# Performance work log

Hardware: AMD Instinct MI355X
Metric: run time of the kernel (lower is better)

The kernel has to match this reference:

```python
import jax, jax.numpy as jnp
import numpy as np
import math

NUM_HEADS = 16
SEGMENT_SIZE = 256
DILATION_RATE = 2


def _hilbert_curve(n):
    if n == 1:
        return [(0, 0)]
    m = n // 2
    sub = _hilbert_curve(m)
    pts = [(y, x) for (x, y) in sub]
    pts += [(x, y + m) for (x, y) in sub]
    pts += [(x + m, y + m) for (x, y) in sub]
    pts += [(m - 1 - y + m, m - 1 - x) for (x, y) in sub]
    return pts


def generate_hilbert_curve_mapping(seq_len):
    grid = 2 ** int(math.ceil(math.log2(math.sqrt(seq_len))))
    pts = _hilbert_curve(grid)
    lin2hil = np.zeros(seq_len, dtype=np.int32)
    for h_idx, (x, y) in enumerate(pts[:seq_len]):
        lin = y * grid + x
        if lin < seq_len:
            lin2hil[lin] = h_idx
    return lin2hil


def setup_inputs() -> dict:
    key = jax.random.key(0)
    k1, k2, k3 = jax.random.split(key, 3)
    B, S, H = 1, 4096, 2048
    scale = H ** -0.5
    x = jax.random.normal(k1, (B, S, H), dtype=jnp.float32)
    w_qkv = jax.random.normal(k2, (3 * H, H), dtype=jnp.float32) * scale
    w_out = jax.random.normal(k3, (H, H), dtype=jnp.float32) * scale
    hilbert_map = jnp.asarray(generate_hilbert_curve_mapping(S))
    return {"x": x, "w_qkv": w_qkv, "w_out": w_out, "hilbert_map": hilbert_map}


def _kv_positions(S, seg, dil):
    # Union of per-segment dilated positions: seg_start + j*dil (< segment end).
    seg_starts = np.arange(0, S, seg)
    within = np.arange(0, seg, dil)
    return jnp.asarray((seg_starts[:, None] + within[None, :]).reshape(-1))


def reference(x, w_qkv, w_out, hilbert_map):
    B, S, H = x.shape
    nh = NUM_HEADS
    hd = H // nh
    qkv = x @ w_qkv.T                              # [B,S,3H]
    qkv = qkv.reshape(B, S, 3, nh, hd).transpose(2, 0, 3, 1, 4)  # [3,B,nh,S,hd]
    q, k, v = qkv[0], qkv[1], qkv[2]

    kv_pos = _kv_positions(S, SEGMENT_SIZE, DILATION_RATE)  # [Nk]
    gathered = hilbert_map[kv_pos]                 # Hilbert-mapped KV indices
    kg = k[:, :, gathered, :]                      # [B,nh,Nk,hd]
    vg = v[:, :, gathered, :]

    scale = 1.0 / jnp.sqrt(jnp.float32(hd))
    scores = jnp.einsum("bhmd,bhnd->bhmn", q, kg) * scale
    p = jax.nn.softmax(scores, axis=-1)
    acc = jnp.einsum("bhmn,bhnd->bhmd", p, vg)     # [B,nh,S,hd]

    # Scatter: out[:, :, hilbert_map[m], :] = acc[:, :, m, :]
    out = jnp.zeros_like(acc).at[:, :, hilbert_map, :].set(acc)
    out = out.transpose(0, 2, 1, 3).reshape(B, S, H)
    return out @ w_out.T
```

## Files before the change

### kernel.cpp

```cpp
#include <hip/hip_runtime.h>
#include <math.h>

#define S_LEN 4096
#define HID   2048
#define NH    16
#define HD    128
#define NKV   2048
#define KT    64
#define QBLK  128
#define NT    (NKV / KT)
#define QSCALE 0.12754103668587426f

typedef __attribute__((ext_vector_type(8))) _Float16 half8;
typedef __attribute__((ext_vector_type(4))) _Float16 half4;
typedef __attribute__((ext_vector_type(2))) __fp16 fp16x2;
typedef __attribute__((ext_vector_type(4))) float f32x4;
typedef __attribute__((ext_vector_type(16))) float f32x16;

#define GLB_AS __attribute__((address_space(1)))
#define LDS_AS __attribute__((address_space(3)))

#if __has_builtin(__builtin_amdgcn_exp2f)
#define EXP2(x) __builtin_amdgcn_exp2f(x)
#else
#define EXP2(x) exp2f(x)
#endif

__device__ __forceinline__ void gload16(const void* g, void* l) {
  __builtin_amdgcn_global_load_lds((GLB_AS const void*)g, (LDS_AS void*)l, 16, 0, 0);
}

__device__ __forceinline__ unsigned pkrtz(float a, float b) {
  union { fp16x2 h; unsigned u; } cv;
  cv.h = __builtin_amdgcn_cvt_pkrtz(a, b);
  return cv.u;
}

__global__ void k_build_idx(const int* __restrict__ hmap, int* __restrict__ gidx) {
  int i = blockIdx.x * 256 + threadIdx.x;
  if (i < NKV) gidx[i] = hmap[2 * i];
}

#define NX8  (S_LEN * HID / 8)
#define NW8  (3 * HID * HID / 8)
#define NO8  (HID * HID / 8)
__global__ void k_cvt_all(const float* __restrict__ x, const float* __restrict__ wq,
                          const float* __restrict__ wo, _Float16* __restrict__ x16,
                          _Float16* __restrict__ wq16, _Float16* __restrict__ wo16) {
  int i = blockIdx.x * 256 + threadIdx.x;
  const float* src; _Float16* dst; int j;
  if (i < NX8)            { src = x;  dst = x16;  j = i; }
  else if (i < NX8 + NW8) { src = wq; dst = wq16; j = i - NX8; }
  else                    { src = wo; dst = wo16; j = i - NX8 - NW8; }
  float4 a = ((const float4*)src)[2 * j];
  float4 b = ((const float4*)src)[2 * j + 1];
  half8 h;
  h[0] = (_Float16)a.x; h[1] = (_Float16)a.y; h[2] = (_Float16)a.z; h[3] = (_Float16)a.w;
  h[4] = (_Float16)b.x; h[5] = (_Float16)b.y; h[6] = (_Float16)b.z; h[7] = (_Float16)b.w;
  ((half8*)dst)[j] = h;
}

__global__ __launch_bounds__(256)
void k_gemm_qkv(const _Float16* __restrict__ A, const _Float16* __restrict__ wqkv,
                _Float16* __restrict__ q16, const int* __restrict__ gidx,
                char* __restrict__ kimg, char* __restrict__ vtimg)
{
  __shared__ __align__(16) char Asl[16384];
  __shared__ __align__(16) char Bsl[16384];
  const int tid = threadIdx.x;
  const int w = tid >> 6, lane = tid & 63;
  const int l15 = lane & 15, l4 = lane >> 4;
  const int wr = w >> 1, wc = w & 1;
  const int K = HID;

  int b = blockIdx.x;
  const bool qpart = b < 512;
  int m0, n0, N;
  const _Float16* B;
  const int* arow;
  if (qpart) { m0 = (b >> 4) * 128; n0 = (b & 15) * 128; N = HID; B = wqkv; arow = nullptr; }
  else { b -= 512; m0 = (b >> 5) * 128; n0 = (b & 31) * 128; N = 2 * HID;
         B = wqkv + (size_t)HID * HID; arow = gidx; }

  const int srow  = lane >> 3;
  const int kso   = ((lane & 7) ^ srow) * 8;
  const _Float16* Ap[4];
  const _Float16* Bp[4];
#pragma unroll
  for (int q = 0; q < 4; ++q) {
    int arel = m0 + 32 * w + 8 * q + srow;
    int ra = arow ? arow[arel] : arel;
    Ap[q] = A + (size_t)ra * K + kso;
    Bp[q] = B + (size_t)(n0 + 32 * w + 8 * q + srow) * K + kso;
  }

  f32x4 acc[4][4];
#pragma unroll
  for (int i = 0; i < 4; ++i)
#pragma unroll
    for (int j = 0; j < 4; ++j) acc[i][j] = (f32x4){0.f, 0.f, 0.f, 0.f};

#define STAGE_T(k0)                                                  \
  do {                                                               \
    _Pragma("unroll")                                                \
    for (int q = 0; q < 4; ++q) {                                    \
      gload16(Ap[q] + (k0), Asl + (4 * w + q) * 1024 + lane * 16);   \
      gload16(Bp[q] + (k0), Bsl + (4 * w + q) * 1024 + lane * 16);   \
    }                                                                \
  } while (0)

  STAGE_T(0);
  __syncthreads();

  const int nt = K >> 6;
  for (int t = 0; t < nt; ++t) {
    half8 af[4][2], bf[4][2];
#pragma unroll
    for (int mi = 0; mi < 4; ++mi) {
      int row = wr * 64 + mi * 16 + l15;
#pragma unroll
      for (int ks = 0; ks < 2; ++ks)
        af[mi][ks] = *(const half8*)(Asl + row * 128 + (((ks * 4 + l4) ^ (row & 7)) * 16));
    }
#pragma unroll
    for (int ni = 0; ni < 4; ++ni) {
      int row = wc * 64 + ni * 16 + l15;
#pragma unroll
      for (int ks = 0; ks < 2; ++ks)
        bf[ni][ks] = *(const half8*)(Bsl + row * 128 + (((ks * 4 + l4) ^ (row & 7)) * 16));
    }
    __syncthreads();
    if (t + 1 < nt) STAGE_T((t + 1) * 64);
    __builtin_amdgcn_s_setprio(1);
#pragma unroll
    for (int mi = 0; mi < 4; ++mi)
#pragma unroll
      for (int ni = 0; ni < 4; ++ni)
#pragma unroll
        for (int ks = 0; ks < 2; ++ks)
          acc[mi][ni] = __builtin_amdgcn_mfma_f32_16x16x32_f16(af[mi][ks], bf[ni][ks], acc[mi][ni], 0, 0, 0);
    __builtin_amdgcn_s_setprio(0);
    __syncthreads();
  }
#undef STAGE_T

  const int rbase = m0 + wr * 64 + l4 * 4;
  const int cbase = n0 + wc * 64 + l15;
#pragma unroll
  for (int mi = 0; mi < 4; ++mi)
#pragma unroll
    for (int ni = 0; ni < 4; ++ni)
#pragma unroll
      for (int e = 0; e < 4; ++e) {
        int row = rbase + mi * 16 + e;
        int col = cbase + ni * 16;
        _Float16 val = (_Float16)acc[mi][ni][e];
        if (qpart) {
          q16[(size_t)row * HID + col] = val;
        } else {
          int t = row >> 6, j = row & 63;
          if (col < HID) {
            int h = col >> 7, d = col & 127;
            int off = (h * 32 + t) * 16384 + ((j * 256 + 2 * d) ^ ((j & 7) << 4));
            *(_Float16*)(kimg + off) = val;
          } else {
            int nn = col - HID;
            int h = nn >> 7, d = nn & 127;
            int off = (h * 32 + t) * 16384 + ((d * 128 + 2 * j) ^ ((d & 7) << 4));
            *(_Float16*)(vtimg + off) = val;
          }
        }
      }
}

__global__ __launch_bounds__(256)
void k_gemm_out(const _Float16* __restrict__ A, const _Float16* __restrict__ B,
                float* __restrict__ C, int M, int N, int K)
{
  __shared__ __align__(16) char Asl[16384];
  __shared__ __align__(16) char Bsl[16384];
  const int tid = threadIdx.x;
  const int w = tid >> 6, lane = tid & 63;
  const int l15 = lane & 15, l4 = lane >> 4;
  const int m0 = blockIdx.y * 128, n0 = blockIdx.x * 128;
  const int wr = w >> 1, wc = w & 1;

  const int srow  = lane >> 3;
  const int kso   = ((lane & 7) ^ srow) * 8;
  const _Float16* Ap[4];
  const _Float16* Bp[4];
#pragma unroll
  for (int q = 0; q < 4; ++q) {
    int row = m0 + 32 * w + 8 * q + srow;
    Ap[q] = A + (size_t)row * K + kso;
    Bp[q] = B + (size_t)(n0 + 32 * w + 8 * q + srow) * K + kso;
  }

  f32x4 acc[4][4];
#pragma unroll
  for (int i = 0; i < 4; ++i)
#pragma unroll
    for (int j = 0; j < 4; ++j) acc[i][j] = (f32x4){0.f, 0.f, 0.f, 0.f};

#define STAGE_T(k0)                                                  \
  do {                                                               \
    _Pragma("unroll")                                                \
    for (int q = 0; q < 4; ++q) {                                    \
      gload16(Ap[q] + (k0), Asl + (4 * w + q) * 1024 + lane * 16);   \
      gload16(Bp[q] + (k0), Bsl + (4 * w + q) * 1024 + lane * 16);   \
    }                                                                \
  } while (0)

  STAGE_T(0);
  __syncthreads();

  const int nt = K >> 6;
  for (int t = 0; t < nt; ++t) {
    half8 af[4][2], bf[4][2];
#pragma unroll
    for (int mi = 0; mi < 4; ++mi) {
      int row = wr * 64 + mi * 16 + l15;
#pragma unroll
      for (int ks = 0; ks < 2; ++ks)
        af[mi][ks] = *(const half8*)(Asl + row * 128 + (((ks * 4 + l4) ^ (row & 7)) * 16));
    }
#pragma unroll
    for (int ni = 0; ni < 4; ++ni) {
      int row = wc * 64 + ni * 16 + l15;
#pragma unroll
      for (int ks = 0; ks < 2; ++ks)
        bf[ni][ks] = *(const half8*)(Bsl + row * 128 + (((ks * 4 + l4) ^ (row & 7)) * 16));
    }
    __syncthreads();
    if (t + 1 < nt) STAGE_T((t + 1) * 64);
    __builtin_amdgcn_s_setprio(1);
#pragma unroll
    for (int mi = 0; mi < 4; ++mi)
#pragma unroll
      for (int ni = 0; ni < 4; ++ni)
#pragma unroll
        for (int ks = 0; ks < 2; ++ks)
          acc[mi][ni] = __builtin_amdgcn_mfma_f32_16x16x32_f16(af[mi][ks], bf[ni][ks], acc[mi][ni], 0, 0, 0);
    __builtin_amdgcn_s_setprio(0);
    __syncthreads();
  }
#undef STAGE_T

  const int rbase = m0 + wr * 64 + l4 * 4;
  const int cbase = n0 + wc * 64 + l15;
#pragma unroll
  for (int mi = 0; mi < 4; ++mi)
#pragma unroll
    for (int ni = 0; ni < 4; ++ni)
#pragma unroll
      for (int e = 0; e < 4; ++e)
        C[(size_t)(rbase + mi * 16 + e) * N + cbase + ni * 16] = acc[mi][ni][e];
}

__global__ __launch_bounds__(256, 2)
void k_attn9(const _Float16* __restrict__ qmat, const char* __restrict__ kimg,
             const char* __restrict__ vtimg, const int* __restrict__ hmap,
             _Float16* __restrict__ att)
{
  extern __shared__ __align__(16) char lds[];
  const int tid = threadIdx.x;
  const int w = tid >> 6, lane = tid & 63;
  const int l31 = lane & 31;
  const bool hi = (lane >> 5) != 0;
  const int hib = hi ? 1 : 0;
  const int work = (blockIdx.x & 7) * 64 + (blockIdx.x >> 3);
  const int h  = work >> 5;
  const int q0 = (work & 31) * QBLK;

  half8 qf[8];
  {
    const int qrow = q0 + w * 32 + l31;
    const _Float16* qb = qmat + (size_t)qrow * HID + h * HD + hib * 8;
    const _Float16 qs = (_Float16)QSCALE;
#pragma unroll
    for (int dk = 0; dk < 8; ++dk) {
      half8 v = *(const half8*)(qb + 16 * dk);
#pragma unroll
      for (int q = 0; q < 8; ++q) v[q] *= qs;
      qf[dk] = v;
    }
  }

  const int swz = (l31 & 7) << 4;
  int koff[4], voff[4];
#pragma unroll
  for (int i = 0; i < 4; ++i) {
    koff[i] = l31 * 256 + ((i * 32 + hib * 16) ^ swz);
    voff[i] = 16384 + l31 * 128 + ((i * 32 + hib * 16) ^ swz);
  }

  const char* kbase = kimg  + (size_t)h * NT * 16384;
  const char* vbase = vtimg + (size_t)h * NT * 16384;

  f32x16 acc[4];
#pragma unroll
  for (int dt = 0; dt < 4; ++dt)
#pragma unroll
    for (int r = 0; r < 16; ++r) acc[dt][r] = 0.f;
  float lsum = 0.f;

#define STAGE(buf, t)                                                          \
  do {                                                                         \
    const char* ks_ = kbase + (size_t)(t) * 16384;                             \
    const char* vs_ = vbase + (size_t)(t) * 16384;                             \
    char* d_ = lds + (buf) * 32768;                                            \
    _Pragma("unroll")                                                          \
    for (int g = 0; g < 4; ++g) {                                              \
      gload16(ks_ + (w + 4 * g) * 1024 + lane * 16, d_ + (w + 4 * g) * 1024);  \
      gload16(vs_ + (w + 4 * g) * 1024 + lane * 16,                            \
              d_ + 16384 + (w + 4 * g) * 1024);                                \
    }                                                                          \
  } while (0)

#define SM_HALF(S, PPK)                                                        \
  do {                                                                         \
    float p_[16];                                                              \
    _Pragma("unroll")                                                          \
    for (int r = 0; r < 16; ++r) { p_[r] = EXP2((S)[r]); lsum += p_[r]; }      \
    _Pragma("unroll")                                                          \
    for (int rq = 0; rq < 4; ++rq)                                             \
      _Pragma("unroll")                                                        \
      for (int h2 = 0; h2 < 2; ++h2)                                           \
        PPK[rq][h2] = pkrtz(p_[4 * rq + 2 * h2], p_[4 * rq + 2 * h2 + 1]);     \
  } while (0)

#define PV_HALF(PPK, KSB, CUR)                                                 \
  do {                                                                         \
    _Pragma("unroll")                                                          \
    for (int k1 = 0; k1 < 2; ++k1) {                                           \
      unsigned send0 = hi ? PPK[2 * k1][0]     : PPK[2 * k1 + 1][0];           \
      unsigned send1 = hi ? PPK[2 * k1][1]     : PPK[2 * k1 + 1][1];           \
      unsigned recv0 = (unsigned)__shfl_xor((int)send0, 32);                   \
      unsigned recv1 = (unsigned)__shfl_xor((int)send1, 32);                   \
      unsigned self0 = hi ? PPK[2 * k1 + 1][0] : PPK[2 * k1][0];               \
      unsigned self1 = hi ? PPK[2 * k1 + 1][1] : PPK[2 * k1][1];               \
      union { unsigned u[4]; half8 hv; } pf;                                   \
      pf.u[0] = hi ? recv0 : self0;                                            \
      pf.u[1] = hi ? recv1 : self1;                                            \
      pf.u[2] = hi ? self0 : recv0;                                            \
      pf.u[3] = hi ? self1 : recv1;                                            \
      __builtin_amdgcn_s_setprio(1);                                           \
      _Pragma("unroll")                                                        \
      for (int dt = 0; dt < 4; ++dt) {                                         \
        half8 vf = *(const half8*)(lds + voff[(KSB) + k1] +                    \
                    ((CUR) * 32768 + dt * 4096));                              \
        acc[dt] = __builtin_amdgcn_mfma_f32_32x32x16_f16(vf, pf.hv, acc[dt], 0, 0, 0); \
      }                                                                        \
      __builtin_amdgcn_s_setprio(0);                                           \
    }                                                                          \
  } while (0)

#define QK_HALF(S, JT, CUR)                                                    \
  do {                                                                         \
    _Pragma("unroll")                                                          \
    for (int r = 0; r < 16; ++r) (S)[r] = 0.f;                                 \
    __builtin_amdgcn_s_setprio(1);                                             \
    _Pragma("unroll")                                                          \
    for (int dk = 0; dk < 8; ++dk) {                                           \
      half8 kf = *(const half8*)(lds + koff[dk & 3] +                          \
                  ((CUR) * 32768 + (JT) * 8192 + (dk >> 2) * 128));            \
      (S) = __builtin_amdgcn_mfma_f32_32x32x16_f16(kf, qf[dk], (S), 0, 0, 0);  \
    }                                                                          \
    __builtin_amdgcn_s_setprio(0);                                             \
  } while (0)

#define TILE(CUR, T)                                                           \
  do {                                                                         \
    if ((T) + 1 < NT) STAGE((CUR) ^ 1, (T) + 1);                               \
    f32x16 sA, sB;                                                             \
    QK_HALF(sA, 0, CUR);                                                       \
    QK_HALF(sB, 1, CUR);                                                       \
    unsigned PA[4][2], PB[4][2];                                               \
    SM_HALF(sA, PA);                                                           \
    PV_HALF(PA, 0, CUR);                                                       \
    SM_HALF(sB, PB);                                                           \
    PV_HALF(PB, 2, CUR);                                                       \
    asm volatile("s_waitcnt vmcnt(0)");                                        \
    __syncthreads();                                                           \
  } while (0)

  STAGE(0, 0);
  asm volatile("s_waitcnt vmcnt(0)");
  __syncthreads();

  for (int t = 0; t < NT; t += 2) {
    TILE(0, t);
    TILE(1, t + 1);
  }
#undef TILE
#undef QK_HALF
#undef PV_HALF
#undef SM_HALF
#undef STAGE

  float lt = lsum + __shfl_xor(lsum, 32);
  const float rl = 1.0f / lt;
  const int qrow = q0 + w * 32 + l31;
  const int srow = hmap[qrow];
  _Float16* ob = att + (size_t)srow * HID + h * HD;
#pragma unroll
  for (int dt = 0; dt < 4; ++dt)
#pragma unroll
    for (int rq = 0; rq < 4; ++rq) {
      const int d0 = dt * 32 + 8 * rq + 4 * hib;
      half4 o;
      o[0] = (_Float16)(acc[dt][4 * rq + 0] * rl);
      o[1] = (_Float16)(acc[dt][4 * rq + 1] * rl);
      o[2] = (_Float16)(acc[dt][4 * rq + 2] * rl);
      o[3] = (_Float16)(acc[dt][4 * rq + 3] * rl);
      *(half4*)(ob + d0) = o;
    }
}

extern "C" void kernel_launch(void* const* d_in, const int* in_sizes, int n_in,
                              void* d_out, int out_size, void* d_ws, size_t ws_size,
                              hipStream_t stream)
{
  const float* x     = (const float*)d_in[0];
  const float* w_qkv = (const float*)d_in[1];
  const float* w_out = (const float*)d_in[2];
  const int*   hmap  = (const int*)d_in[3];
  float* out = (float*)d_out;

  char* ws = (char*)d_ws;
  int* gidx = (int*)ws;                                          ws += 8192;
  _Float16* x16    = (_Float16*)ws;
  _Float16* att16  = (_Float16*)ws;                              ws += (size_t)S_LEN * HID * 2;
  _Float16* wqkv16 = (_Float16*)ws;                              ws += (size_t)3 * HID * HID * 2;
  _Float16* wout16 = (_Float16*)ws;                              ws += (size_t)HID * HID * 2;
  _Float16* q16    = (_Float16*)ws;                              ws += (size_t)S_LEN * HID * 2;
  char* kimg  = ws;                                              ws += (size_t)NH * NT * 16384;
  char* vtimg = ws;

  k_build_idx<<<8, 256, 0, stream>>>(hmap, gidx);
  k_cvt_all<<<(NX8 + NW8 + NO8 + 255) / 256, 256, 0, stream>>>(x, w_qkv, w_out,
                                                               x16, wqkv16, wout16);

  k_gemm_qkv<<<1024, 256, 0, stream>>>(x16, wqkv16, q16, gidx, kimg, vtimg);

  k_attn9<<<NH * (S_LEN / QBLK), 256, 65536, stream>>>(q16, kimg, vtimg, hmap, att16);

  dim3 go(HID / 128, S_LEN / 128);
  k_gemm_out<<<go, 256, 0, stream>>>(att16, wout16, out, S_LEN, HID, HID);
}
```

Before: 224.5 us.

## Use 512-thread attention blocks with 4-stage KV ring and software-pipelined QK

The attention kernel now runs 8 waves per block over 256 query rows, so each staged K/V tile is shared by twice as many queries. The LDS double buffer becomes a four-slot ring that prefetches three tiles ahead, with partial vmcnt waits. The QK product for the next tile is interleaved with softmax and PV of the current tile to overlap MFMA work. This needs 128KB of LDS per block, which with launch_bounds(512,2) may limit residency and increase register pressure from the extra in-flight score tiles.

```diff
diff --git a/kernel.cpp b/kernel.cpp
--- a/kernel.cpp
+++ b/kernel.cpp
@@ -7,7 +7,7 @@
 #define HD    128
 #define NKV   2048
 #define KT    64
-#define QBLK  128
+#define QBLK  256
 #define NT    (NKV / KT)
 #define QSCALE 0.12754103668587426f
 
@@ -257,10 +257,10 @@
         C[(size_t)(rbase + mi * 16 + e) * N + cbase + ni * 16] = acc[mi][ni][e];
 }
 
-__global__ __launch_bounds__(256, 2)
-void k_attn9(const _Float16* __restrict__ qmat, const char* __restrict__ kimg,
-             const char* __restrict__ vtimg, const int* __restrict__ hmap,
-             _Float16* __restrict__ att)
+__global__ __launch_bounds__(512, 2)
+void k_attn10(const _Float16* __restrict__ qmat, const char* __restrict__ kimg,
+              const char* __restrict__ vtimg, const int* __restrict__ hmap,
+              _Float16* __restrict__ att)
 {
   extern __shared__ __align__(16) char lds[];
   const int tid = threadIdx.x;
@@ -268,9 +268,9 @@
   const int l31 = lane & 31;
   const bool hi = (lane >> 5) != 0;
   const int hib = hi ? 1 : 0;
-  const int work = (blockIdx.x & 7) * 64 + (blockIdx.x >> 3);
-  const int h  = work >> 5;
-  const int q0 = (work & 31) * QBLK;
+  const int work = (blockIdx.x & 7) * 32 + (blockIdx.x >> 3);
+  const int h  = work >> 4;
+  const int q0 = (work & 15) * QBLK;
 
   half8 qf[8];
   {
@@ -309,12 +309,10 @@
     const char* ks_ = kbase + (size_t)(t) * 16384;                             \
     const char* vs_ = vbase + (size_t)(t) * 16384;                             \
     char* d_ = lds + (buf) * 32768;                                            \
-    _Pragma("unroll")                                                          \
-    for (int g = 0; g < 4; ++g) {                                              \
-      gload16(ks_ + (w + 4 * g) * 1024 + lane * 16, d_ + (w + 4 * g) * 1024);  \
-      gload16(vs_ + (w + 4 * g) * 1024 + lane * 16,                            \
-              d_ + 16384 + (w + 4 * g) * 1024);                                \
-    }                                                                          \
+    gload16(ks_ + w * 1024 + lane * 16,          d_ + w * 1024);               \
+    gload16(ks_ + (8 + w) * 1024 + lane * 16,    d_ + (8 + w) * 1024);         \
+    gload16(vs_ + w * 1024 + lane * 16,          d_ + 16384 + w * 1024);       \
+    gload16(vs_ + (8 + w) * 1024 + lane * 16,    d_ + 16384 + (8 + w) * 1024); \
   } while (0)
 
 #define SM_HALF(S, PPK)                                                        \
@@ -329,7 +327,7 @@
         PPK[rq][h2] = pkrtz(p_[4 * rq + 2 * h2], p_[4 * rq + 2 * h2 + 1]);     \
   } while (0)
 
-#define PV_HALF(PPK, KSB, CUR)                                                 \
+#define PV_HALF(PPK, KSB, BUF)                                                 \
   do {                                                                         \
     _Pragma("unroll")                                                          \
     for (int k1 = 0; k1 < 2; ++k1) {                                           \
@@ -348,14 +346,14 @@
       _Pragma("unroll")                                                        \
       for (int dt = 0; dt < 4; ++dt) {                                         \
         half8 vf = *(const half8*)(lds + voff[(KSB) + k1] +                    \
-                    ((CUR) * 32768 + dt * 4096));                              \
+                    ((BUF) * 32768 + dt * 4096));                              \
         acc[dt] = __builtin_amdgcn_mfma_f32_32x32x16_f16(vf, pf.hv, acc[dt], 0, 0, 0); \
       }                                                                        \
       __builtin_amdgcn_s_setprio(0);                                           \
     }                                                                          \
   } while (0)
 
-#define QK_HALF(S, JT, CUR)                                                    \
+#define QK_HALF(S, JT, BUF)                                                    \
   do {                                                                         \
     _Pragma("unroll")                                                          \
     for (int r = 0; r < 16; ++r) (S)[r] = 0.f;                                 \
@@ -363,35 +361,46 @@
     _Pragma("unroll")                                                          \
     for (int dk = 0; dk < 8; ++dk) {                                           \
       half8 kf = *(const half8*)(lds + koff[dk & 3] +                          \
-                  ((CUR) * 32768 + (JT) * 8192 + (dk >> 2) * 128));            \
+                  ((BUF) * 32768 + (JT) * 8192 + (dk >> 2) * 128));            \
       (S) = __builtin_amdgcn_mfma_f32_32x32x16_f16(kf, qf[dk], (S), 0, 0, 0);  \
     }                                                                          \
     __builtin_amdgcn_s_setprio(0);                                             \
   } while (0)
 
-#define TILE(CUR, T)                                                           \
+#define TILE(CUR, T, DOSTAGE, DOQK, WAITASM)                                   \
   do {                                                                         \
-    if ((T) + 1 < NT) STAGE((CUR) ^ 1, (T) + 1);                               \
-    f32x16 sA, sB;                                                             \
-    QK_HALF(sA, 0, CUR);                                                       \
-    QK_HALF(sB, 1, CUR);                                                       \
+    if (DOSTAGE) STAGE((((CUR) + 3) & 3), (T) + 3);                            \
     unsigned PA[4][2], PB[4][2];                                               \
     SM_HALF(sA, PA);                                                           \
-    PV_HALF(PA, 0, CUR);                                                       \
+    if (DOQK) QK_HALF(sA, 0, (((CUR) + 1) & 3));                               \
+    PV_HALF(PA, 0, (CUR));                                                     \
     SM_HALF(sB, PB);                                                           \
-    PV_HALF(PB, 2, CUR);                                                       \
-    asm volatile("s_waitcnt vmcnt(0)");                                        \
-    __syncthreads();                                                           \
+    if (DOQK) QK_HALF(sB, 1, (((CUR) + 1) & 3));                               \
+    PV_HALF(PB, 2, (CUR));                                                     \
+    asm volatile(WAITASM ::: "memory");                                        \
+    __builtin_amdgcn_s_barrier();                                              \
   } while (0)
 
   STAGE(0, 0);
-  asm volatile("s_waitcnt vmcnt(0)");
-  __syncthreads();
-
-  for (int t = 0; t < NT; t += 2) {
-    TILE(0, t);
-    TILE(1, t + 1);
-  }
+  STAGE(1, 1);
+  STAGE(2, 2);
+  asm volatile("s_waitcnt vmcnt(4)" ::: "memory");
+  __builtin_amdgcn_s_barrier();
+
+  f32x16 sA, sB;
+  QK_HALF(sA, 0, 0);
+  QK_HALF(sB, 1, 0);
+
+  for (int t = 0; t < 28; t += 4) {
+    TILE(0, t + 0, true, true, "s_waitcnt vmcnt(4)");
+    TILE(1, t + 1, true, true, "s_waitcnt vmcnt(4)");
+    TILE(2, t + 2, true, true, "s_waitcnt vmcnt(4)");
+    TILE(3, t + 3, true, true, "s_waitcnt vmcnt(4)");
+  }
+  TILE(0, 28, true,  true,  "s_waitcnt vmcnt(4)");
+  TILE(1, 29, false, true,  "s_waitcnt vmcnt(0)");
+  TILE(2, 30, false, true,  "s_waitcnt vmcnt(0)");
+  TILE(3, 31, false, false, "s_waitcnt vmcnt(0)");
 #undef TILE
 #undef QK_HALF
 #undef PV_HALF
@@ -443,7 +452,7 @@
 
   k_gemm_qkv<<<1024, 256, 0, stream>>>(x16, wqkv16, q16, gidx, kimg, vtimg);
 
-  k_attn9<<<NH * (S_LEN / QBLK), 256, 65536, stream>>>(q16, kimg, vtimg, hmap, att16);
+  k_attn10<<<NH * (S_LEN / QBLK), 512, 131072, stream>>>(q16, kimg, vtimg, hmap, att16);
 
   dim3 go(HID / 128, S_LEN / 128);
   k_gemm_out<<<go, 256, 0, stream>>>(att16, wout16, out, S_LEN, HID, HID);
```

Measured after the change: 217.9 us. 1.03x faster.
